# Performance work log

Hardware: AMD Instinct MI355X
Metric: run time of the kernel (lower is better)

Reference implementation:

```python
import jax, jax.numpy as jnp
import numpy as np

N = 50000
E = 800000
DES, TW, NUMP, CATP = 768, 768, 4, 3
EMB = 384
THIRD = EMB // 3  # 128


def _lin(key, fan_in, fan_out):
    k1, k2 = jax.random.split(key)
    bound = 1.0 / np.sqrt(fan_in)
    W = jax.random.uniform(k1, (fan_in, fan_out), jnp.float32, -bound, bound)
    b = jax.random.uniform(k2, (fan_out,), jnp.float32, -bound, bound)
    return W, b


def setup_inputs() -> dict:
    key = jax.random.key(0)
    ks = jax.random.split(key, 16)
    des = jax.random.normal(ks[0], (N, DES), jnp.float32)
    tweet = jax.random.normal(ks[1], (N, TW), jnp.float32)
    num_prop = jax.random.normal(ks[2], (N, NUMP), jnp.float32)
    cat_prop = jax.random.normal(ks[3], (N, CATP), jnp.float32)
    edge_index = jax.random.randint(ks[4], (2, E), 0, N, jnp.int64)
    W_des, b_des = _lin(ks[5], DES, THIRD)
    W_num, b_num = _lin(ks[6], NUMP, THIRD)
    W_cat, b_cat = _lin(ks[7], CATP, THIRD)
    W_in, b_in = _lin(ks[8], EMB, EMB)
    W_g1, b_g1 = _lin(ks[9], EMB, EMB)
    W_g2, b_g2 = _lin(ks[10], EMB, EMB)
    W_o1, b_o1 = _lin(ks[11], EMB, EMB)
    W_o2, b_o2 = _lin(ks[12], EMB, 2)
    return dict(des=des, tweet=tweet, num_prop=num_prop, cat_prop=cat_prop,
                edge_index=edge_index,
                W_des=W_des, b_des=b_des, W_num=W_num, b_num=b_num,
                W_cat=W_cat, b_cat=b_cat, W_in=W_in, b_in=b_in,
                W_g1=W_g1, b_g1=b_g1, W_g2=W_g2, b_g2=b_g2,
                W_o1=W_o1, b_o1=b_o1, W_o2=W_o2, b_o2=b_o2)


def _leaky(x):
    return jax.nn.leaky_relu(x, 0.01)


def _gcn_conv(x, edge_index, W, b):
    # PyG GCNConv: x' = D^{-1/2} (A + I) D^{-1/2} (x W) + b
    src, dst = edge_index[0], edge_index[1]
    x = x @ W  # [N, out]
    n = x.shape[0]
    deg = jax.ops.segment_sum(jnp.ones(src.shape[0], x.dtype), dst, num_segments=n) + 1.0  # self-loop
    dinv = jax.lax.rsqrt(deg)  # deg >= 1
    norm = dinv[src] * dinv[dst]  # [E]
    msg = x[src] * norm[:, None]  # [E, out] gather
    agg = jax.ops.segment_sum(msg, dst, num_segments=n)  # scatter-add
    agg = agg + x * (dinv * dinv)[:, None]  # self-loop contribution
    return agg + b


def reference(des, tweet, num_prop, cat_prop, edge_index,
              W_des, b_des, W_num, b_num, W_cat, b_cat, W_in, b_in,
              W_g1, b_g1, W_g2, b_g2, W_o1, b_o1, W_o2, b_o2):
    # eval mode: dropout is identity
    d = _leaky(des @ W_des + b_des)
    n = _leaky(num_prop @ W_num + b_num)
    c = _leaky(cat_prop @ W_cat + b_cat)
    x = jnp.concatenate((d, n, c), axis=1)  # [N, EMB]
    x = _leaky(x @ W_in + b_in)
    x = _gcn_conv(x, edge_index, W_g1, b_g1)
    x = _gcn_conv(x, edge_index, W_g2, b_g2)
    x = _leaky(x @ W_o1 + b_o1)
    return x @ W_o2 + b_o2  # [N, 2]
```

## Files before the change

kernel.cpp:

```cpp
#include <hip/hip_runtime.h>
#include <hip/hip_bf16.h>
#include <cstdint>

#define NFEAT 384
#define DESK 768
#define THIRD 128

typedef __bf16 bf16x8 __attribute__((ext_vector_type(8)));
typedef unsigned short u16x8 __attribute__((ext_vector_type(8)));
typedef unsigned short u16x4 __attribute__((ext_vector_type(4)));
typedef float f32x16 __attribute__((ext_vector_type(16)));

__device__ __forceinline__ float leaky(float x) { return x > 0.f ? x : 0.01f * x; }

__device__ __forceinline__ unsigned short bfhi(float x) {
  unsigned int u = __float_as_uint(x);
  u += 0x7fffu + ((u >> 16) & 1u);
  return (unsigned short)(u >> 16);
}
__device__ __forceinline__ float bf2f(unsigned short h) {
  return __uint_as_float(((unsigned int)h) << 16);
}
__device__ __forceinline__ void bsplit(float x, unsigned short& h,
                                       unsigned short& l) {
  h = bfhi(x);
  l = bfhi(x - bf2f(h));
}

#define MFMA(a, b, c) __builtin_amdgcn_mfma_f32_32x32x16_bf16(a, b, c, 0, 0, 0)

template <int AFP32, int EPI>
__global__ __launch_bounds__(256, 2) void mfma_gemm(
    const float* __restrict__ Af, const unsigned short* __restrict__ Ahi,
    const unsigned short* __restrict__ Alo,
    const unsigned short* __restrict__ BThi,
    const unsigned short* __restrict__ BTlo, float* __restrict__ Cf,
    unsigned short* __restrict__ Chi, unsigned short* __restrict__ Clo,
    const float* __restrict__ bias, int M, int K, int ldc) {
  __shared__ unsigned short AhiL[4 * 128 * 8];
  __shared__ unsigned short AloL[4 * 128 * 8];
  __shared__ unsigned short BhiL[4 * 128 * 8];
  __shared__ unsigned short BloL[4 * 128 * 8];
  const int tid = threadIdx.x;
  const int lane = tid & 63;
  const int w = tid >> 6;
  const int wm = (w >> 1) * 64, wn = (w & 1) * 64;
  const int lm = lane & 31, lk = lane >> 5;
  const int m_base = blockIdx.x * 128, n_base = blockIdx.y * 128;
  f32x16 a00 = {0.f, 0.f, 0.f, 0.f, 0.f, 0.f, 0.f, 0.f,
                0.f, 0.f, 0.f, 0.f, 0.f, 0.f, 0.f, 0.f};
  f32x16 a01 = a00, a10 = a00, a11 = a00;

  for (int kt = 0; kt < K; kt += 32) {
    if (AFP32) {
#pragma unroll
      for (int it = 0; it < 4; it++) {
        int r = (tid >> 3) + it * 32;
        int q = tid & 7;
        int gr = m_base + r;
        float4 av = make_float4(0.f, 0.f, 0.f, 0.f);
        if (gr < M) av = *(const float4*)&Af[(size_t)gr * K + kt + q * 4];
        unsigned short h0, h1, h2, h3, l0, l1, l2, l3;
        bsplit(av.x, h0, l0);
        bsplit(av.y, h1, l1);
        bsplit(av.z, h2, l2);
        bsplit(av.w, h3, l3);
        int base = ((q >> 1) * 128 + r) * 8 + (q & 1) * 4;
        u16x4 th;
        th.x = h0; th.y = h1; th.z = h2; th.w = h3;
        u16x4 tl;
        tl.x = l0; tl.y = l1; tl.z = l2; tl.w = l3;
        *(u16x4*)&AhiL[base] = th;
        *(u16x4*)&AloL[base] = tl;
      }
    } else {
#pragma unroll
      for (int it = 0; it < 2; it++) {
        int r = (tid >> 2) + it * 64;
        int kb = tid & 3;
        int gr = m_base + r;
        u16x8 vh = {0, 0, 0, 0, 0, 0, 0, 0};
        u16x8 vl = {0, 0, 0, 0, 0, 0, 0, 0};
        if (gr < M) {
          vh = *(const u16x8*)&Ahi[(size_t)gr * K + kt + kb * 8];
          vl = *(const u16x8*)&Alo[(size_t)gr * K + kt + kb * 8];
        }
        *(u16x8*)&AhiL[(kb * 128 + r) * 8] = vh;
        *(u16x8*)&AloL[(kb * 128 + r) * 8] = vl;
      }
    }
#pragma unroll
    for (int it = 0; it < 2; it++) {
      int n = (tid >> 2) + it * 64;
      int kb = tid & 3;
      *(u16x8*)&BhiL[(kb * 128 + n) * 8] =
          *(const u16x8*)&BThi[(size_t)(n_base + n) * K + kt + kb * 8];
      *(u16x8*)&BloL[(kb * 128 + n) * 8] =
          *(const u16x8*)&BTlo[(size_t)(n_base + n) * K + kt + kb * 8];
    }
    __syncthreads();
#pragma unroll
    for (int ks = 0; ks < 2; ks++) {
      int kb = 2 * ks + lk;
      bf16x8 ah0 = __builtin_bit_cast(
          bf16x8, *(const u16x8*)&AhiL[(kb * 128 + wm + lm) * 8]);
      bf16x8 ah1 = __builtin_bit_cast(
          bf16x8, *(const u16x8*)&AhiL[(kb * 128 + wm + 32 + lm) * 8]);
      bf16x8 al0 = __builtin_bit_cast(
          bf16x8, *(const u16x8*)&AloL[(kb * 128 + wm + lm) * 8]);
      bf16x8 al1 = __builtin_bit_cast(
          bf16x8, *(const u16x8*)&AloL[(kb * 128 + wm + 32 + lm) * 8]);
      bf16x8 bh0 = __builtin_bit_cast(
          bf16x8, *(const u16x8*)&BhiL[(kb * 128 + wn + lm) * 8]);
      bf16x8 bh1 = __builtin_bit_cast(
          bf16x8, *(const u16x8*)&BhiL[(kb * 128 + wn + 32 + lm) * 8]);
      bf16x8 bl0 = __builtin_bit_cast(
          bf16x8, *(const u16x8*)&BloL[(kb * 128 + wn + lm) * 8]);
      bf16x8 bl1 = __builtin_bit_cast(
          bf16x8, *(const u16x8*)&BloL[(kb * 128 + wn + 32 + lm) * 8]);
      a00 = MFMA(ah0, bh0, a00);
      a01 = MFMA(ah0, bh1, a01);
      a10 = MFMA(ah1, bh0, a10);
      a11 = MFMA(ah1, bh1, a11);
      a00 = MFMA(ah0, bl0, a00);
      a01 = MFMA(ah0, bl1, a01);
      a10 = MFMA(ah1, bl0, a10);
      a11 = MFMA(ah1, bl1, a11);
      a00 = MFMA(al0, bh0, a00);
      a01 = MFMA(al0, bh1, a01);
      a10 = MFMA(al1, bh0, a10);
      a11 = MFMA(al1, bh1, a11);
    }
    __syncthreads();
  }
  const int colb = n_base + wn;
#pragma unroll
  for (int mt = 0; mt < 2; mt++) {
#pragma unroll
    for (int nt = 0; nt < 2; nt++) {
      f32x16 v = (mt == 0) ? (nt == 0 ? a00 : a01) : (nt == 0 ? a10 : a11);
      int col = colb + nt * 32 + lm;
      float bv = (EPI == 0) ? bias[col] : 0.f;
      int rb = m_base + wm + mt * 32 + 4 * lk;
#pragma unroll
      for (int rg = 0; rg < 16; rg++) {
        int row = rb + (rg & 3) + 8 * (rg >> 2);
        if (row < M) {
          float x = v[rg];
          if (EPI == 0) {
            x = leaky(x + bv);
            unsigned short h, l;
            bsplit(x, h, l);
            Chi[(size_t)row * ldc + col] = h;
            Clo[(size_t)row * ldc + col] = l;
          } else {
            Cf[(size_t)row * ldc + col] = x;
          }
        }
      }
    }
  }
}

__global__ __launch_bounds__(256) void split_transpose(
    const float* __restrict__ src, unsigned short* __restrict__ dsthi,
    unsigned short* __restrict__ dstlo, int R, int C) {
  __shared__ float tile[32][33];
  int tx = threadIdx.x & 31, ty = threadIdx.x >> 5;
  int c0 = blockIdx.x * 32, r0 = blockIdx.y * 32;
#pragma unroll
  for (int i = 0; i < 4; i++)
    tile[ty + i * 8][tx] = src[(size_t)(r0 + ty + i * 8) * C + c0 + tx];
  __syncthreads();
#pragma unroll
  for (int i = 0; i < 4; i++) {
    int c = c0 + ty + i * 8, r = r0 + tx;
    float v = tile[tx][ty + i * 8];
    unsigned short h, l;
    bsplit(v, h, l);
    dsthi[(size_t)c * R + r] = h;
    dstlo[(size_t)c * R + r] = l;
  }
}

__global__ __launch_bounds__(256) void gemm384(const float* __restrict__ A,
                                               const float* __restrict__ B,
                                               float* __restrict__ C) {
  __shared__ float As[16][68];
  __shared__ float Bs[16][64];
  const int tid = threadIdx.x;
  const int mb = blockIdx.x * 64;
  const int nb = blockIdx.y * 64;
  float acc[4][4] = {};
  const int arow = tid >> 2, akq = tid & 3;
  const int brow = tid >> 4, bc4 = tid & 15;
  const int m0 = (tid >> 4) * 4, n0 = (tid & 15) * 4;
  for (int kk = 0; kk < 384; kk += 16) {
    float4 av = *(const float4*)&A[(mb + arow) * 384 + kk + akq * 4];
    As[akq * 4 + 0][arow] = av.x;
    As[akq * 4 + 1][arow] = av.y;
    As[akq * 4 + 2][arow] = av.z;
    As[akq * 4 + 3][arow] = av.w;
    *(float4*)&Bs[brow][bc4 * 4] =
        *(const float4*)&B[(kk + brow) * 384 + nb + bc4 * 4];
    __syncthreads();
#pragma unroll
    for (int k = 0; k < 16; k++) {
      float4 a4 = *(const float4*)&As[k][m0];
      float4 b4 = *(const float4*)&Bs[k][n0];
      float a[4] = {a4.x, a4.y, a4.z, a4.w};
      float b[4] = {b4.x, b4.y, b4.z, b4.w};
#pragma unroll
      for (int i = 0; i < 4; i++)
#pragma unroll
        for (int j = 0; j < 4; j++) acc[i][j] = fmaf(a[i], b[j], acc[i][j]);
    }
    __syncthreads();
  }
#pragma unroll
  for (int i = 0; i < 4; i++)
#pragma unroll
    for (int j = 0; j < 4; j++)
      C[(mb + m0 + i) * 384 + nb + n0 + j] = acc[i][j];
}

__global__ void uv_kernel(const float* __restrict__ T1,
                          const float* __restrict__ W_o1,
                          const float* __restrict__ b_g1,
                          const float* __restrict__ b_g2,
                          const float* __restrict__ b_o1, float* __restrict__ u,
                          float* __restrict__ v) {
  int j = blockIdx.x * blockDim.x + threadIdx.x;
  if (j < 384) {
    float su = 0.f, sv = 0.f;
    for (int k = 0; k < 384; k++) {
      su = fmaf(T1[k * 384 + j], b_g1[k], su);
      sv = fmaf(W_o1[k * 384 + j], b_g2[k], sv);
    }
    u[j] = su;
    v[j] = sv + b_o1[j];
  }
}

__global__ __launch_bounds__(256) void numcat_kernel(
    const float* __restrict__ num, const float* __restrict__ cat,
    const float* __restrict__ Wn, const float* __restrict__ bn,
    const float* __restrict__ Wc, const float* __restrict__ bc,
    unsigned short* __restrict__ x0hi, unsigned short* __restrict__ x0lo) {
  int i = blockIdx.x;
  int c = threadIdx.x;
  float val;
  if (c < 128) {
    val = bn[c];
    val = fmaf(num[i * 4 + 0], Wn[0 * 128 + c], val);
    val = fmaf(num[i * 4 + 1], Wn[1 * 128 + c], val);
    val = fmaf(num[i * 4 + 2], Wn[2 * 128 + c], val);
    val = fmaf(num[i * 4 + 3], Wn[3 * 128 + c], val);
  } else {
    int cc = c - 128;
    val = bc[cc];
    val = fmaf(cat[i * 3 + 0], Wc[0 * 128 + cc], val);
    val = fmaf(cat[i * 3 + 1], Wc[1 * 128 + cc], val);
    val = fmaf(cat[i * 3 + 2], Wc[2 * 128 + cc], val);
  }
  val = leaky(val);
  unsigned short h, l;
  bsplit(val, h, l);
  size_t o = (size_t)i * NFEAT + 128 + c;
  x0hi[o] = h;
  x0lo[o] = l;
}

__global__ void count_kernel(const int* __restrict__ dst, int* __restrict__ deg,
                             int E) {
  int e = blockIdx.x * blockDim.x + threadIdx.x;
  if (e < E) atomicAdd(&deg[dst[e]], 1);
}

__global__ void scan_reduce(const int* __restrict__ deg,
                            int* __restrict__ partial, int N) {
  __shared__ int sm[512];
  int i = blockIdx.x * 512 + threadIdx.x;
  sm[threadIdx.x] = (i < N) ? deg[i] : 0;
  __syncthreads();
  for (int off = 256; off; off >>= 1) {
    if (threadIdx.x < off) sm[threadIdx.x] += sm[threadIdx.x + off];
    __syncthreads();
  }
  if (threadIdx.x == 0) partial[blockIdx.x] = sm[0];
}

__global__ void scan_top(int* partial, int nb) {
  if (threadIdx.x == 0 && blockIdx.x == 0) {
    int run = 0;
    for (int b = 0; b < nb; b++) {
      int t = partial[b];
      partial[b] = run;
      run += t;
    }
  }
}

__global__ void scan_down(const int* __restrict__ deg,
                          const int* __restrict__ partial,
                          int* __restrict__ offsets, int* __restrict__ cursor,
                          int N, int E) {
  __shared__ int sm[512];
  int t = threadIdx.x;
  int i = blockIdx.x * 512 + t;
  int val = (i < N) ? deg[i] : 0;
  sm[t] = val;
  __syncthreads();
  for (int off = 1; off < 512; off <<= 1) {
    int add = (t >= off) ? sm[t - off] : 0;
    __syncthreads();
    sm[t] += add;
    __syncthreads();
  }
  if (i < N) {
    int ex = partial[blockIdx.x] + sm[t] - val;
    offsets[i] = ex;
    cursor[i] = ex;
  }
  if (i == 0) offsets[N] = E;
}

__global__ void dinv_kernel(const int* __restrict__ deg,
                            float* __restrict__ dinv, int N) {
  int i = blockIdx.x * blockDim.x + threadIdx.x;
  if (i < N) dinv[i] = 1.0f / sqrtf((float)deg[i] + 1.0f);
}

__global__ void fill_kernel(const int* __restrict__ src,
                            const int* __restrict__ dst,
                            int* __restrict__ cursor,
                            int* __restrict__ csr_off,
                            float* __restrict__ csr_w,
                            const float* __restrict__ dinv, int E) {
  int e = blockIdx.x * blockDim.x + threadIdx.x;
  if (e < E) {
    int s = src[e], d = dst[e];
    int slot = atomicAdd(&cursor[d], 1);
    csr_off[slot] = s * NFEAT;
    csr_w[slot] = dinv[s] * dinv[d];
  }
}

template <int WRITE_S, int FINAL>
__global__ __launch_bounds__(192) void agg_kernel(
    const float* __restrict__ xin, float* __restrict__ xout,
    const int* __restrict__ offsets, const int* __restrict__ csr_off,
    const float* __restrict__ csr_w, const float* __restrict__ dinv,
    float* __restrict__ sout, const float* __restrict__ svec,
    const float* __restrict__ uvec, const float* __restrict__ vvec,
    const float* __restrict__ W_o2, const float* __restrict__ b_o2,
    float* __restrict__ out) {
  int i = blockIdx.x;
  int t = threadIdx.x;
  int ff = 2 * t;
  int beg = offsets[i], end = offsets[i + 1];
  float di = dinv[i];
  float dii = di * di;
  float2 xs = *(const float2*)&xin[(size_t)i * NFEAT + ff];
  float A0x = dii * xs.x, A0y = dii * xs.y;
  float A1x = 0.f, A1y = 0.f, A2x = 0.f, A2y = 0.f, A3x = 0.f, A3y = 0.f;
  float wsum = dii;
  __shared__ int ssrc[192];
  __shared__ float sw[192];
  for (int j0 = beg; j0 < end; j0 += 192) {
    int cnt = min(192, end - j0);
    if (t < cnt) {
      ssrc[t] = csr_off[j0 + t];
      sw[t] = csr_w[j0 + t];
    }
    __syncthreads();
    int j = 0;
    for (; j + 8 <= cnt; j += 8) {
      int o0 = ssrc[j + 0], o1 = ssrc[j + 1], o2 = ssrc[j + 2],
          o3 = ssrc[j + 3];
      int o4 = ssrc[j + 4], o5 = ssrc[j + 5], o6 = ssrc[j + 6],
          o7 = ssrc[j + 7];
      float w0 = sw[j + 0], w1 = sw[j + 1], w2 = sw[j + 2], w3 = sw[j + 3];
      float w4 = sw[j + 4], w5 = sw[j + 5], w6 = sw[j + 6], w7 = sw[j + 7];
      float2 v0 = *(const float2*)&xin[o0 + ff];
      float2 v1 = *(const float2*)&xin[o1 + ff];
      float2 v2 = *(const float2*)&xin[o2 + ff];
      float2 v3 = *(const float2*)&xin[o3 + ff];
      float2 v4 = *(const float2*)&xin[o4 + ff];
      float2 v5 = *(const float2*)&xin[o5 + ff];
      float2 v6 = *(const float2*)&xin[o6 + ff];
      float2 v7 = *(const float2*)&xin[o7 + ff];
      A0x = fmaf(w0, v0.x, A0x);
      A0y = fmaf(w0, v0.y, A0y);
      A1x = fmaf(w1, v1.x, A1x);
      A1y = fmaf(w1, v1.y, A1y);
      A2x = fmaf(w2, v2.x, A2x);
      A2y = fmaf(w2, v2.y, A2y);
      A3x = fmaf(w3, v3.x, A3x);
      A3y = fmaf(w3, v3.y, A3y);
      A0x = fmaf(w4, v4.x, A0x);
      A0y = fmaf(w4, v4.y, A0y);
      A1x = fmaf(w5, v5.x, A1x);
      A1y = fmaf(w5, v5.y, A1y);
      A2x = fmaf(w6, v6.x, A2x);
      A2y = fmaf(w6, v6.y, A2y);
      A3x = fmaf(w7, v7.x, A3x);
      A3y = fmaf(w7, v7.y, A3y);
      if (WRITE_S) wsum += ((w0 + w1) + (w2 + w3)) + ((w4 + w5) + (w6 + w7));
    }
    for (; j < cnt; j++) {
      float wj = sw[j];
      float2 vj = *(const float2*)&xin[ssrc[j] + ff];
      A0x = fmaf(wj, vj.x, A0x);
      A0y = fmaf(wj, vj.y, A0y);
      if (WRITE_S) wsum += wj;
    }
    __syncthreads();
  }
  float ax = (A0x + A1x) + (A2x + A3x);
  float ay = (A0y + A1y) + (A2y + A3y);
  if (!FINAL) {
    float2 r;
    r.x = ax;
    r.y = ay;
    *(float2*)&xout[(size_t)i * NFEAT + ff] = r;
    if (WRITE_S && t == 0) sout[i] = wsum;
  } else {
    float si = svec[i];
    float v0 = leaky(ax + si * uvec[ff + 0] + vvec[ff + 0]);
    float v1 = leaky(ay + si * uvec[ff + 1] + vvec[ff + 1]);
    float c0 = v0 * W_o2[(ff + 0) * 2 + 0] + v1 * W_o2[(ff + 1) * 2 + 0];
    float c1 = v0 * W_o2[(ff + 0) * 2 + 1] + v1 * W_o2[(ff + 1) * 2 + 1];
#pragma unroll
    for (int off2 = 32; off2; off2 >>= 1) {
      c0 += __shfl_down(c0, off2, 64);
      c1 += __shfl_down(c1, off2, 64);
    }
    __shared__ float red[3][2];
    int wid = t >> 6, lane2 = t & 63;
    if (lane2 == 0) {
      red[wid][0] = c0;
      red[wid][1] = c1;
    }
    __syncthreads();
    if (t == 0) {
      out[i * 2 + 0] = red[0][0] + red[1][0] + red[2][0] + b_o2[0];
      out[i * 2 + 1] = red[0][1] + red[1][1] + red[2][1] + b_o2[1];
    }
  }
}

extern "C" void kernel_launch(void* const* d_in, const int* in_sizes, int n_in,
                              void* d_out, int out_size, void* d_ws,
                              size_t ws_size, hipStream_t stream) {
  const float* des = (const float*)d_in[0];
  const float* num_prop = (const float*)d_in[2];
  const float* cat_prop = (const float*)d_in[3];
  const int* edge = (const int*)d_in[4];
  const float* W_des = (const float*)d_in[5];
  const float* b_des = (const float*)d_in[6];
  const float* W_num = (const float*)d_in[7];
  const float* b_num = (const float*)d_in[8];
  const float* W_cat = (const float*)d_in[9];
  const float* b_cat = (const float*)d_in[10];
  const float* W_in = (const float*)d_in[11];
  const float* b_in = (const float*)d_in[12];
  const float* W_g1 = (const float*)d_in[13];
  const float* b_g1 = (const float*)d_in[14];
  const float* W_g2 = (const float*)d_in[15];
  const float* b_g2 = (const float*)d_in[16];
  const float* W_o1 = (const float*)d_in[17];
  const float* b_o1 = (const float*)d_in[18];
  const float* W_o2 = (const float*)d_in[19];
  const float* b_o2 = (const float*)d_in[20];
  float* out = (float*)d_out;

  const int N = in_sizes[0] / DESK;
  const int E = in_sizes[4] / 2;
  const int* esrc = edge;
  const int* edst = edge + E;

  char* ws = (char*)d_ws;
  size_t off = 0;
  auto alloc = [&](size_t n) {
    off = (off + 255) & ~(size_t)255;
    size_t o = off;
    off += n;
    return o;
  };
  float* bufA = (float*)(ws + alloc((size_t)N * NFEAT * 4));
  float* bufB = (float*)(ws + alloc((size_t)N * NFEAT * 4));
  int* deg = (int*)(ws + alloc((size_t)N * 4));
  int* offsets = (int*)(ws + alloc((size_t)(N + 1) * 4));
  int* cursor = (int*)(ws + alloc((size_t)N * 4));
  int* partial = (int*)(ws + alloc(1024 * 4));
  float* dinv = (float*)(ws + alloc((size_t)N * 4));
  float* svec = (float*)(ws + alloc((size_t)N * 4));
  int* csr_off = (int*)(ws + alloc((size_t)E * 4));
  float* csr_w = (float*)(ws + alloc((size_t)E * 4));
  float* T1 = (float*)(ws + alloc(384 * 384 * 4));
  float* Mmat = (float*)(ws + alloc(384 * 384 * 4));
  float* uvec = (float*)(ws + alloc(384 * 4));
  float* vvec = (float*)(ws + alloc(384 * 4));
  unsigned short* WdThi = (unsigned short*)(ws + alloc(768 * 128 * 2));
  unsigned short* WdTlo = (unsigned short*)(ws + alloc(768 * 128 * 2));
  unsigned short* WiThi = (unsigned short*)(ws + alloc(384 * 384 * 2));
  unsigned short* WiTlo = (unsigned short*)(ws + alloc(384 * 384 * 2));
  unsigned short* MmThi = (unsigned short*)(ws + alloc(384 * 384 * 2));
  unsigned short* MmTlo = (unsigned short*)(ws + alloc(384 * 384 * 2));
  (void)ws_size;
  (void)n_in;
  (void)out_size;

  unsigned short* x0hi = (unsigned short*)bufA;
  unsigned short* x0lo = x0hi + (size_t)N * NFEAT;
  unsigned short* x1hi = (unsigned short*)bufB;
  unsigned short* x1lo = x1hi + (size_t)N * NFEAT;
  float* yb = bufA;
  float* w1 = bufB;

  hipMemsetAsync(deg, 0, (size_t)N * 4, stream);

  dim3 g6(6, 6);
  gemm384<<<g6, 256, 0, stream>>>(W_g2, W_o1, T1);
  gemm384<<<g6, 256, 0, stream>>>(W_g1, T1, Mmat);
  uv_kernel<<<2, 256, 0, stream>>>(T1, W_o1, b_g1, b_g2, b_o1, uvec, vvec);
  split_transpose<<<dim3(4, 24), 256, 0, stream>>>(W_des, WdThi, WdTlo, 768,
                                                   128);
  split_transpose<<<dim3(12, 12), 256, 0, stream>>>(W_in, WiThi, WiTlo, 384,
                                                    384);
  split_transpose<<<dim3(12, 12), 256, 0, stream>>>(Mmat, MmThi, MmTlo, 384,
                                                    384);

  const int MT = (N + 127) / 128;
  mfma_gemm<1, 0><<<dim3(MT, 1), 256, 0, stream>>>(
      des, nullptr, nullptr, WdThi, WdTlo, nullptr, x0hi, x0lo, b_des, N, DESK,
      NFEAT);
  numcat_kernel<<<N, 256, 0, stream>>>(num_prop, cat_prop, W_num, b_num, W_cat,
                                       b_cat, x0hi, x0lo);
  mfma_gemm<0, 0><<<dim3(MT, 3), 256, 0, stream>>>(
      nullptr, x0hi, x0lo, WiThi, WiTlo, nullptr, x1hi, x1lo, b_in, N, NFEAT,
      NFEAT);
  mfma_gemm<0, 1><<<dim3(MT, 3), 256, 0, stream>>>(
      nullptr, x1hi, x1lo, MmThi, MmTlo, yb, nullptr, nullptr, nullptr, N,
      NFEAT, NFEAT);

  const int EB = (E + 255) / 256;
  count_kernel<<<EB, 256, 0, stream>>>(edst, deg, E);
  const int NB = (N + 511) / 512;
  scan_reduce<<<NB, 512, 0, stream>>>(deg, partial, N);
  scan_top<<<1, 64, 0, stream>>>(partial, NB);
  scan_down<<<NB, 512, 0, stream>>>(deg, partial, offsets, cursor, N, E);
  dinv_kernel<<<(N + 255) / 256, 256, 0, stream>>>(deg, dinv, N);
  fill_kernel<<<EB, 256, 0, stream>>>(esrc, edst, cursor, csr_off, csr_w, dinv,
                                      E);

  agg_kernel<1, 0><<<N, 192, 0, stream>>>(yb, w1, offsets, csr_off, csr_w, dinv,
                                          svec, nullptr, nullptr, nullptr,
                                          nullptr, nullptr, nullptr);
  agg_kernel<0, 1><<<N, 192, 0, stream>>>(w1, nullptr, offsets, csr_off, csr_w,
                                          dinv, nullptr, svec, uvec, vvec, W_o2,
                                          b_o2, out);
}
```

Measured before the change: 1.094 ms.

## Store aggregation features in fp16, persistent-grid agg/numcat, merge small kernels

Result: faster. 960.0 us (-12.2%).

```diff
diff --git a/kernel.cpp b/kernel.cpp
--- a/kernel.cpp
+++ b/kernel.cpp
@@ -10,6 +10,7 @@
 typedef unsigned short u16x8 __attribute__((ext_vector_type(8)));
 typedef unsigned short u16x4 __attribute__((ext_vector_type(4)));
 typedef float f32x16 __attribute__((ext_vector_type(16)));
+typedef _Float16 h16x2 __attribute__((ext_vector_type(2)));
 
 __device__ __forceinline__ float leaky(float x) { return x > 0.f ? x : 0.01f * x; }
 
@@ -34,7 +35,7 @@
     const float* __restrict__ Af, const unsigned short* __restrict__ Ahi,
     const unsigned short* __restrict__ Alo,
     const unsigned short* __restrict__ BThi,
-    const unsigned short* __restrict__ BTlo, float* __restrict__ Cf,
+    const unsigned short* __restrict__ BTlo, _Float16* __restrict__ Ch16,
     unsigned short* __restrict__ Chi, unsigned short* __restrict__ Clo,
     const float* __restrict__ bias, int M, int K, int ldc) {
   __shared__ unsigned short AhiL[4 * 128 * 8];
@@ -154,7 +155,7 @@
             Chi[(size_t)row * ldc + col] = h;
             Clo[(size_t)row * ldc + col] = l;
           } else {
-            Cf[(size_t)row * ldc + col] = x;
+            Ch16[(size_t)row * ldc + col] = (_Float16)x;
           }
         }
       }
@@ -162,12 +163,22 @@
   }
 }
 
-__global__ __launch_bounds__(256) void split_transpose(
-    const float* __restrict__ src, unsigned short* __restrict__ dsthi,
-    unsigned short* __restrict__ dstlo, int R, int C) {
+__global__ __launch_bounds__(256) void split_transpose_b(
+    const float* __restrict__ s0, unsigned short* __restrict__ h0,
+    unsigned short* __restrict__ l0, const float* __restrict__ s1,
+    unsigned short* __restrict__ h1, unsigned short* __restrict__ l1,
+    const float* __restrict__ s2, unsigned short* __restrict__ h2,
+    unsigned short* __restrict__ l2) {
+  int z = blockIdx.z;
+  const float* src = z == 0 ? s0 : (z == 1 ? s1 : s2);
+  unsigned short* dsthi = z == 0 ? h0 : (z == 1 ? h1 : h2);
+  unsigned short* dstlo = z == 0 ? l0 : (z == 1 ? l1 : l2);
+  int R = z == 0 ? 768 : 384;
+  int C = z == 0 ? 128 : 384;
+  int c0 = blockIdx.x * 32, r0 = blockIdx.y * 32;
+  if (c0 >= C || r0 >= R) return;
   __shared__ float tile[32][33];
   int tx = threadIdx.x & 31, ty = threadIdx.x >> 5;
-  int c0 = blockIdx.x * 32, r0 = blockIdx.y * 32;
 #pragma unroll
   for (int i = 0; i < 4; i++)
     tile[ty + i * 8][tx] = src[(size_t)(r0 + ty + i * 8) * C + c0 + tx];
@@ -246,29 +257,31 @@
     const float* __restrict__ num, const float* __restrict__ cat,
     const float* __restrict__ Wn, const float* __restrict__ bn,
     const float* __restrict__ Wc, const float* __restrict__ bc,
-    unsigned short* __restrict__ x0hi, unsigned short* __restrict__ x0lo) {
-  int i = blockIdx.x;
+    unsigned short* __restrict__ x0hi, unsigned short* __restrict__ x0lo,
+    int N) {
   int c = threadIdx.x;
-  float val;
-  if (c < 128) {
-    val = bn[c];
-    val = fmaf(num[i * 4 + 0], Wn[0 * 128 + c], val);
-    val = fmaf(num[i * 4 + 1], Wn[1 * 128 + c], val);
-    val = fmaf(num[i * 4 + 2], Wn[2 * 128 + c], val);
-    val = fmaf(num[i * 4 + 3], Wn[3 * 128 + c], val);
-  } else {
-    int cc = c - 128;
-    val = bc[cc];
-    val = fmaf(cat[i * 3 + 0], Wc[0 * 128 + cc], val);
-    val = fmaf(cat[i * 3 + 1], Wc[1 * 128 + cc], val);
-    val = fmaf(cat[i * 3 + 2], Wc[2 * 128 + cc], val);
-  }
-  val = leaky(val);
-  unsigned short h, l;
-  bsplit(val, h, l);
-  size_t o = (size_t)i * NFEAT + 128 + c;
-  x0hi[o] = h;
-  x0lo[o] = l;
+  for (int i = blockIdx.x; i < N; i += gridDim.x) {
+    float val;
+    if (c < 128) {
+      val = bn[c];
+      val = fmaf(num[i * 4 + 0], Wn[0 * 128 + c], val);
+      val = fmaf(num[i * 4 + 1], Wn[1 * 128 + c], val);
+      val = fmaf(num[i * 4 + 2], Wn[2 * 128 + c], val);
+      val = fmaf(num[i * 4 + 3], Wn[3 * 128 + c], val);
+    } else {
+      int cc = c - 128;
+      val = bc[cc];
+      val = fmaf(cat[i * 3 + 0], Wc[0 * 128 + cc], val);
+      val = fmaf(cat[i * 3 + 1], Wc[1 * 128 + cc], val);
+      val = fmaf(cat[i * 3 + 2], Wc[2 * 128 + cc], val);
+    }
+    val = leaky(val);
+    unsigned short h, l;
+    bsplit(val, h, l);
+    size_t o = (size_t)i * NFEAT + 128 + c;
+    x0hi[o] = h;
+    x0lo[o] = l;
+  }
 }
 
 __global__ void count_kernel(const int* __restrict__ dst, int* __restrict__ deg,
@@ -304,7 +317,7 @@
 __global__ void scan_down(const int* __restrict__ deg,
                           const int* __restrict__ partial,
                           int* __restrict__ offsets, int* __restrict__ cursor,
-                          int N, int E) {
+                          float* __restrict__ dinv, int N, int E) {
   __shared__ int sm[512];
   int t = threadIdx.x;
   int i = blockIdx.x * 512 + t;
@@ -321,14 +334,9 @@
     int ex = partial[blockIdx.x] + sm[t] - val;
     offsets[i] = ex;
     cursor[i] = ex;
+    dinv[i] = 1.0f / sqrtf((float)val + 1.0f);
   }
   if (i == 0) offsets[N] = E;
-}
-
-__global__ void dinv_kernel(const int* __restrict__ deg,
-                            float* __restrict__ dinv, int N) {
-  int i = blockIdx.x * blockDim.x + threadIdx.x;
-  if (i < N) dinv[i] = 1.0f / sqrtf((float)deg[i] + 1.0f);
 }
 
 __global__ void fill_kernel(const int* __restrict__ src,
@@ -348,104 +356,119 @@
 
 template <int WRITE_S, int FINAL>
 __global__ __launch_bounds__(192) void agg_kernel(
-    const float* __restrict__ xin, float* __restrict__ xout,
+    const _Float16* __restrict__ xin, _Float16* __restrict__ xout,
     const int* __restrict__ offsets, const int* __restrict__ csr_off,
     const float* __restrict__ csr_w, const float* __restrict__ dinv,
     float* __restrict__ sout, const float* __restrict__ svec,
     const float* __restrict__ uvec, const float* __restrict__ vvec,
     const float* __restrict__ W_o2, const float* __restrict__ b_o2,
-    float* __restrict__ out) {
-  int i = blockIdx.x;
-  int t = threadIdx.x;
-  int ff = 2 * t;
-  int beg = offsets[i], end = offsets[i + 1];
-  float di = dinv[i];
-  float dii = di * di;
-  float2 xs = *(const float2*)&xin[(size_t)i * NFEAT + ff];
-  float A0x = dii * xs.x, A0y = dii * xs.y;
-  float A1x = 0.f, A1y = 0.f, A2x = 0.f, A2y = 0.f, A3x = 0.f, A3y = 0.f;
-  float wsum = dii;
+    float* __restrict__ out, int N) {
+  const int t = threadIdx.x;
+  const int ff = 2 * t;
   __shared__ int ssrc[192];
   __shared__ float sw[192];
-  for (int j0 = beg; j0 < end; j0 += 192) {
-    int cnt = min(192, end - j0);
-    if (t < cnt) {
-      ssrc[t] = csr_off[j0 + t];
-      sw[t] = csr_w[j0 + t];
-    }
-    __syncthreads();
-    int j = 0;
-    for (; j + 8 <= cnt; j += 8) {
-      int o0 = ssrc[j + 0], o1 = ssrc[j + 1], o2 = ssrc[j + 2],
-          o3 = ssrc[j + 3];
-      int o4 = ssrc[j + 4], o5 = ssrc[j + 5], o6 = ssrc[j + 6],
-          o7 = ssrc[j + 7];
-      float w0 = sw[j + 0], w1 = sw[j + 1], w2 = sw[j + 2], w3 = sw[j + 3];
-      float w4 = sw[j + 4], w5 = sw[j + 5], w6 = sw[j + 6], w7 = sw[j + 7];
-      float2 v0 = *(const float2*)&xin[o0 + ff];
-      float2 v1 = *(const float2*)&xin[o1 + ff];
-      float2 v2 = *(const float2*)&xin[o2 + ff];
-      float2 v3 = *(const float2*)&xin[o3 + ff];
-      float2 v4 = *(const float2*)&xin[o4 + ff];
-      float2 v5 = *(const float2*)&xin[o5 + ff];
-      float2 v6 = *(const float2*)&xin[o6 + ff];
-      float2 v7 = *(const float2*)&xin[o7 + ff];
-      A0x = fmaf(w0, v0.x, A0x);
-      A0y = fmaf(w0, v0.y, A0y);
-      A1x = fmaf(w1, v1.x, A1x);
-      A1y = fmaf(w1, v1.y, A1y);
-      A2x = fmaf(w2, v2.x, A2x);
-      A2y = fmaf(w2, v2.y, A2y);
-      A3x = fmaf(w3, v3.x, A3x);
-      A3y = fmaf(w3, v3.y, A3y);
-      A0x = fmaf(w4, v4.x, A0x);
-      A0y = fmaf(w4, v4.y, A0y);
-      A1x = fmaf(w5, v5.x, A1x);
-      A1y = fmaf(w5, v5.y, A1y);
-      A2x = fmaf(w6, v6.x, A2x);
-      A2y = fmaf(w6, v6.y, A2y);
-      A3x = fmaf(w7, v7.x, A3x);
-      A3y = fmaf(w7, v7.y, A3y);
-      if (WRITE_S) wsum += ((w0 + w1) + (w2 + w3)) + ((w4 + w5) + (w6 + w7));
-    }
-    for (; j < cnt; j++) {
-      float wj = sw[j];
-      float2 vj = *(const float2*)&xin[ssrc[j] + ff];
-      A0x = fmaf(wj, vj.x, A0x);
-      A0y = fmaf(wj, vj.y, A0y);
-      if (WRITE_S) wsum += wj;
-    }
-    __syncthreads();
-  }
-  float ax = (A0x + A1x) + (A2x + A3x);
-  float ay = (A0y + A1y) + (A2y + A3y);
-  if (!FINAL) {
-    float2 r;
-    r.x = ax;
-    r.y = ay;
-    *(float2*)&xout[(size_t)i * NFEAT + ff] = r;
-    if (WRITE_S && t == 0) sout[i] = wsum;
-  } else {
-    float si = svec[i];
-    float v0 = leaky(ax + si * uvec[ff + 0] + vvec[ff + 0]);
-    float v1 = leaky(ay + si * uvec[ff + 1] + vvec[ff + 1]);
-    float c0 = v0 * W_o2[(ff + 0) * 2 + 0] + v1 * W_o2[(ff + 1) * 2 + 0];
-    float c1 = v0 * W_o2[(ff + 0) * 2 + 1] + v1 * W_o2[(ff + 1) * 2 + 1];
-#pragma unroll
-    for (int off2 = 32; off2; off2 >>= 1) {
-      c0 += __shfl_down(c0, off2, 64);
-      c1 += __shfl_down(c1, off2, 64);
-    }
-    __shared__ float red[3][2];
-    int wid = t >> 6, lane2 = t & 63;
-    if (lane2 == 0) {
-      red[wid][0] = c0;
-      red[wid][1] = c1;
-    }
-    __syncthreads();
-    if (t == 0) {
-      out[i * 2 + 0] = red[0][0] + red[1][0] + red[2][0] + b_o2[0];
-      out[i * 2 + 1] = red[0][1] + red[1][1] + red[2][1] + b_o2[1];
+  __shared__ float red[3][2];
+  float u0 = 0.f, u1 = 0.f, vc0 = 0.f, vc1 = 0.f;
+  float w00 = 0.f, w01 = 0.f, w10 = 0.f, w11 = 0.f, bo0 = 0.f, bo1 = 0.f;
+  if (FINAL) {
+    u0 = uvec[ff];
+    u1 = uvec[ff + 1];
+    vc0 = vvec[ff];
+    vc1 = vvec[ff + 1];
+    w00 = W_o2[ff * 2 + 0];
+    w01 = W_o2[ff * 2 + 1];
+    w10 = W_o2[(ff + 1) * 2 + 0];
+    w11 = W_o2[(ff + 1) * 2 + 1];
+    bo0 = b_o2[0];
+    bo1 = b_o2[1];
+  }
+  for (int i = blockIdx.x; i < N; i += gridDim.x) {
+    int beg = offsets[i], end = offsets[i + 1];
+    float di = dinv[i];
+    float dii = di * di;
+    h16x2 xs = *(const h16x2*)&xin[(size_t)i * NFEAT + ff];
+    float A0x = dii * (float)xs.x, A0y = dii * (float)xs.y;
+    float A1x = 0.f, A1y = 0.f, A2x = 0.f, A2y = 0.f, A3x = 0.f, A3y = 0.f;
+    float wsum = dii;
+    for (int j0 = beg; j0 < end; j0 += 192) {
+      int cnt = min(192, end - j0);
+      if (t < cnt) {
+        ssrc[t] = csr_off[j0 + t];
+        sw[t] = csr_w[j0 + t];
+      }
+      __syncthreads();
+      int j = 0;
+      for (; j + 8 <= cnt; j += 8) {
+        int o0 = ssrc[j + 0], o1 = ssrc[j + 1], o2 = ssrc[j + 2],
+            o3 = ssrc[j + 3];
+        int o4 = ssrc[j + 4], o5 = ssrc[j + 5], o6 = ssrc[j + 6],
+            o7 = ssrc[j + 7];
+        float w0 = sw[j + 0], w1 = sw[j + 1], w2 = sw[j + 2], w3 = sw[j + 3];
+        float w4 = sw[j + 4], w5 = sw[j + 5], w6 = sw[j + 6], w7 = sw[j + 7];
+        h16x2 v0 = *(const h16x2*)&xin[o0 + ff];
+        h16x2 v1 = *(const h16x2*)&xin[o1 + ff];
+        h16x2 v2 = *(const h16x2*)&xin[o2 + ff];
+        h16x2 v3 = *(const h16x2*)&xin[o3 + ff];
+        h16x2 v4 = *(const h16x2*)&xin[o4 + ff];
+        h16x2 v5 = *(const h16x2*)&xin[o5 + ff];
+        h16x2 v6 = *(const h16x2*)&xin[o6 + ff];
+        h16x2 v7 = *(const h16x2*)&xin[o7 + ff];
+        A0x = fmaf(w0, (float)v0.x, A0x);
+        A0y = fmaf(w0, (float)v0.y, A0y);
+        A1x = fmaf(w1, (float)v1.x, A1x);
+        A1y = fmaf(w1, (float)v1.y, A1y);
+        A2x = fmaf(w2, (float)v2.x, A2x);
+        A2y = fmaf(w2, (float)v2.y, A2y);
+        A3x = fmaf(w3, (float)v3.x, A3x);
+        A3y = fmaf(w3, (float)v3.y, A3y);
+        A0x = fmaf(w4, (float)v4.x, A0x);
+        A0y = fmaf(w4, (float)v4.y, A0y);
+        A1x = fmaf(w5, (float)v5.x, A1x);
+        A1y = fmaf(w5, (float)v5.y, A1y);
+        A2x = fmaf(w6, (float)v6.x, A2x);
+        A2y = fmaf(w6, (float)v6.y, A2y);
+        A3x = fmaf(w7, (float)v7.x, A3x);
+        A3y = fmaf(w7, (float)v7.y, A3y);
+        if (WRITE_S) wsum += ((w0 + w1) + (w2 + w3)) + ((w4 + w5) + (w6 + w7));
+      }
+      for (; j < cnt; j++) {
+        float wj = sw[j];
+        h16x2 vj = *(const h16x2*)&xin[ssrc[j] + ff];
+        A0x = fmaf(wj, (float)vj.x, A0x);
+        A0y = fmaf(wj, (float)vj.y, A0y);
+        if (WRITE_S) wsum += wj;
+      }
+      __syncthreads();
+    }
+    float ax = (A0x + A1x) + (A2x + A3x);
+    float ay = (A0y + A1y) + (A2y + A3y);
+    if (!FINAL) {
+      h16x2 r;
+      r.x = (_Float16)ax;
+      r.y = (_Float16)ay;
+      *(h16x2*)&xout[(size_t)i * NFEAT + ff] = r;
+      if (WRITE_S && t == 0) sout[i] = wsum;
+    } else {
+      float si = svec[i];
+      float q0 = leaky(ax + si * u0 + vc0);
+      float q1 = leaky(ay + si * u1 + vc1);
+      float c0 = q0 * w00 + q1 * w10;
+      float c1 = q0 * w01 + q1 * w11;
+#pragma unroll
+      for (int off2 = 32; off2; off2 >>= 1) {
+        c0 += __shfl_down(c0, off2, 64);
+        c1 += __shfl_down(c1, off2, 64);
+      }
+      int wid = t >> 6, lane2 = t & 63;
+      if (lane2 == 0) {
+        red[wid][0] = c0;
+        red[wid][1] = c1;
+      }
+      __syncthreads();
+      if (t == 0) {
+        out[i * 2 + 0] = red[0][0] + red[1][0] + red[2][0] + bo0;
+        out[i * 2 + 1] = red[0][1] + red[1][1] + red[2][1] + bo1;
+      }
     }
   }
 }
@@ -516,8 +539,8 @@
   unsigned short* x0lo = x0hi + (size_t)N * NFEAT;
   unsigned short* x1hi = (unsigned short*)bufB;
   unsigned short* x1lo = x1hi + (size_t)N * NFEAT;
-  float* yb = bufA;
-  float* w1 = bufB;
+  _Float16* yb = (_Float16*)bufA;
+  _Float16* w1 = (_Float16*)bufB;
 
   hipMemsetAsync(deg, 0, (size_t)N * 4, stream);
 
@@ -525,19 +548,15 @@
   gemm384<<<g6, 256, 0, stream>>>(W_g2, W_o1, T1);
   gemm384<<<g6, 256, 0, stream>>>(W_g1, T1, Mmat);
   uv_kernel<<<2, 256, 0, stream>>>(T1, W_o1, b_g1, b_g2, b_o1, uvec, vvec);
-  split_transpose<<<dim3(4, 24), 256, 0, stream>>>(W_des, WdThi, WdTlo, 768,
-                                                   128);
-  split_transpose<<<dim3(12, 12), 256, 0, stream>>>(W_in, WiThi, WiTlo, 384,
-                                                    384);
-  split_transpose<<<dim3(12, 12), 256, 0, stream>>>(Mmat, MmThi, MmTlo, 384,
-                                                    384);
+  split_transpose_b<<<dim3(12, 24, 3), 256, 0, stream>>>(
+      W_des, WdThi, WdTlo, W_in, WiThi, WiTlo, Mmat, MmThi, MmTlo);
 
   const int MT = (N + 127) / 128;
   mfma_gemm<1, 0><<<dim3(MT, 1), 256, 0, stream>>>(
       des, nullptr, nullptr, WdThi, WdTlo, nullptr, x0hi, x0lo, b_des, N, DESK,
       NFEAT);
-  numcat_kernel<<<N, 256, 0, stream>>>(num_prop, cat_prop, W_num, b_num, W_cat,
-                                       b_cat, x0hi, x0lo);
+  numcat_kernel<<<1024, 256, 0, stream>>>(num_prop, cat_prop, W_num, b_num,
+                                          W_cat, b_cat, x0hi, x0lo, N);
   mfma_gemm<0, 0><<<dim3(MT, 3), 256, 0, stream>>>(
       nullptr, x0hi, x0lo, WiThi, WiTlo, nullptr, x1hi, x1lo, b_in, N, NFEAT,
       NFEAT);
@@ -550,15 +569,14 @@
   const int NB = (N + 511) / 512;
   scan_reduce<<<NB, 512, 0, stream>>>(deg, partial, N);
   scan_top<<<1, 64, 0, stream>>>(partial, NB);
-  scan_down<<<NB, 512, 0, stream>>>(deg, partial, offsets, cursor, N, E);
-  dinv_kernel<<<(N + 255) / 256, 256, 0, stream>>>(deg, dinv, N);
+  scan_down<<<NB, 512, 0, stream>>>(deg, partial, offsets, cursor, dinv, N, E);
   fill_kernel<<<EB, 256, 0, stream>>>(esrc, edst, cursor, csr_off, csr_w, dinv,
                                       E);
 
-  agg_kernel<1, 0><<<N, 192, 0, stream>>>(yb, w1, offsets, csr_off, csr_w, dinv,
-                                          svec, nullptr, nullptr, nullptr,
-                                          nullptr, nullptr, nullptr);
-  agg_kernel<0, 1><<<N, 192, 0, stream>>>(w1, nullptr, offsets, csr_off, csr_w,
-                                          dinv, nullptr, svec, uvec, vvec, W_o2,
-                                          b_o2, out);
-}
+  agg_kernel<1, 0><<<4096, 192, 0, stream>>>(
+      yb, w1, offsets, csr_off, csr_w, dinv, svec, nullptr, nullptr, nullptr,
+      nullptr, nullptr, nullptr, N);
+  agg_kernel<0, 1><<<4096, 192, 0, stream>>>(
+      w1, nullptr, offsets, csr_off, csr_w, dinv, nullptr, svec, uvec, vvec,
+      W_o2, b_o2, out, N);
+}
```
